# Kernel tuning notes

Measured on AMD Instinct MI355X. Metric: run time of the kernel, lower is better.

The kernel has to match this reference:

```python
import jax, jax.numpy as jnp
import numpy as np

BN_EPS = 1e-3  # Keras BatchNormalization default epsilon


def setup_inputs() -> dict:
    key = jax.random.key(0)
    ks = jax.random.split(key, 16)
    B, N, M = 4, 16384, 4096
    C1, C2 = 128, 256
    mlp = [256, 128]
    cin = C2 + C1
    inp = {
        "xyz1": jax.random.normal(ks[0], (B, N, 3), dtype=jnp.float32),
        "xyz2": jax.random.normal(ks[1], (B, M, 3), dtype=jnp.float32),
        "points1": jax.random.normal(ks[2], (B, N, C1), dtype=jnp.float32),
        "points2": jax.random.normal(ks[3], (B, M, C2), dtype=jnp.float32),
    }
    k = 4
    for i, cout in enumerate(mlp):
        inp[f"w{i}"] = jax.random.normal(ks[k], (cin, cout), dtype=jnp.float32) * (1.0 / np.sqrt(cin)); k += 1
        inp[f"g{i}"] = jnp.ones((cout,), dtype=jnp.float32) + 0.1 * jax.random.normal(ks[k], (cout,), dtype=jnp.float32); k += 1
        inp[f"b{i}"] = 0.1 * jax.random.normal(ks[k], (cout,), dtype=jnp.float32); k += 1
        inp[f"m{i}"] = 0.1 * jax.random.normal(ks[k], (cout,), dtype=jnp.float32); k += 1
        inp[f"v{i}"] = 0.5 + jax.random.uniform(ks[k], (cout,), dtype=jnp.float32); k += 1
        cin = cout
    return inp


def _three_nn(xyz1, xyz2):
    # squared pairwise distances [B,N,M] via ||a||^2 + ||b||^2 - 2ab
    n1 = jnp.sum(xyz1 * xyz1, axis=-1)                      # [B,N]
    n2 = jnp.sum(xyz2 * xyz2, axis=-1)                      # [B,M]
    d2 = n1[:, :, None] + n2[:, None, :] - 2.0 * jnp.einsum("bnc,bmc->bnm", xyz1, xyz2)
    d2 = jnp.maximum(d2, 0.0)
    neg, idx = jax.lax.top_k(-d2, 3)                        # 3 smallest distances
    return -neg, idx                                        # dist [B,N,3], idx [B,N,3]


def reference(xyz1, xyz2, points1, points2,
              w0, g0, b0, m0, v0, w1, g1, b1, m1, v1):
    dist, idx = _three_nn(xyz1, xyz2)
    dist = jnp.maximum(dist, 1e-10)
    inv = 1.0 / dist                                        # [B,N,3]
    weight = inv / jnp.sum(inv, axis=2, keepdims=True)      # [B,N,3]
    # three_interpolate: irregular gather + weighted sum
    gathered = jax.vmap(lambda p, i: p[i])(points2, idx)    # [B,N,3,C2]
    interp = jnp.einsum("bnk,bnkc->bnc", weight, gathered)  # [B,N,C2]
    x = jnp.concatenate([interp, points1], axis=2)          # [B,N,C2+C1]
    # 1x1 Conv2D (no bias) + BN(inference) + ReLU stack
    for w, g, b, m, v in ((w0, g0, b0, m0, v0), (w1, g1, b1, m1, v1)):
        x = jnp.einsum("bnc,cd->bnd", x, w)
        x = (x - m) * (g * jax.lax.rsqrt(v + BN_EPS)) + b
        x = jax.nn.relu(x)
    return x
```

## Files before the change

kernel.cpp:

```cpp
#include <hip/hip_runtime.h>
#include <hip/hip_bf16.h>

typedef __bf16 bf16x8 __attribute__((ext_vector_type(8)));
typedef float  f32x4  __attribute__((ext_vector_type(4)));
typedef unsigned short ushort_t;
typedef unsigned int   uint_t;

__device__ __forceinline__ ushort_t f2bf(float f) {
    union { float f; uint_t u; } v; v.f = f;
    uint_t r = v.u + 0x7fffu + ((v.u >> 16) & 1u);
    return (ushort_t)(r >> 16);
}

__device__ __forceinline__ void async_copy16(const void* g, void* l) {
    __builtin_amdgcn_global_load_lds(
        (const __attribute__((address_space(1))) unsigned int*)g,
        (__attribute__((address_space(3))) unsigned int*)l, 16, 0, 0);
}

#define BATCH 4
#define NPTS  16384
#define MPTS  4096
#define C1    128
#define C2    256
#define NCHUNK 4
#define CHUNK  (MPTS / NCHUNK)

__global__ __launch_bounds__(256) void prep_kernel(
    const float* __restrict__ w0, const float* __restrict__ w1,
    const float* __restrict__ g0, const float* __restrict__ b0,
    const float* __restrict__ m0, const float* __restrict__ v0,
    const float* __restrict__ g1, const float* __restrict__ b1,
    const float* __restrict__ m1, const float* __restrict__ v1,
    ushort_t* __restrict__ wt0, ushort_t* __restrict__ wt1,
    float* __restrict__ sc0, float* __restrict__ sh0,
    float* __restrict__ sc1, float* __restrict__ sh1) {
    int i = blockIdx.x * 256 + threadIdx.x;
    if (i < 256 * 384) {
        int n = i / 384, k = i % 384;
        wt0[i] = f2bf(w0[k * 256 + n]);
    }
    if (i < 128 * 256) {
        int n = i / 256, k = i % 256;
        wt1[i] = f2bf(w1[k * 128 + n]);
    }
    if (i < 256) { float s = g0[i] * rsqrtf(v0[i] + 1e-3f); sc0[i] = s; sh0[i] = b0[i] - m0[i] * s; }
    if (i < 128) { float s = g1[i] * rsqrtf(v1[i] + 1e-3f); sc1[i] = s; sh1[i] = b1[i] - m1[i] * s; }
}

__global__ __launch_bounds__(256) void knn_partial(
    const float* __restrict__ xyz1, const float* __restrict__ xyz2,
    float* __restrict__ pd, int* __restrict__ pi) {
    __shared__ __align__(16) float sx[CHUNK], sy_[CHUNK], sz[CHUNK], sw[CHUNK];
    const int t  = threadIdx.x;
    const int qb = blockIdx.x;
    const int c  = blockIdx.y;
    const int b  = blockIdx.z;
#pragma unroll
    for (int j = 0; j < CHUNK / 256; j++) {
        const int m = j * 256 + t;
        const float* g = xyz2 + ((long)b * MPTS + c * CHUNK + m) * 3;
        const float x = g[0], y = g[1], z = g[2];
        sx[m] = x; sy_[m] = y; sz[m] = z; sw[m] = x * x + y * y + z * z;
    }
    __syncthreads();
    const int n = qb * 256 + t;
    const long base = ((long)b * NPTS + n) * 3;
    const float qx = xyz1[base], qy = xyz1[base + 1], qz = xyz1[base + 2];
    const float nx = -2.f * qx, ny = -2.f * qy, nz = -2.f * qz;
    float d0 = 3.4e38f, d1 = 3.4e38f, d2 = 3.4e38f;
    int   i0 = 0, i1 = 0, i2 = 0;
    const int mb = c * CHUNK;
    for (int g = 0; g < CHUNK; g += 4) {
        const float4 X = *(const float4*)&sx[g];
        const float4 Y = *(const float4*)&sy_[g];
        const float4 Z = *(const float4*)&sz[g];
        const float4 W = *(const float4*)&sw[g];
        const float xs[4] = {X.x, X.y, X.z, X.w};
        const float ys[4] = {Y.x, Y.y, Y.z, Y.w};
        const float zs[4] = {Z.x, Z.y, Z.z, Z.w};
        const float ws[4] = {W.x, W.y, W.z, W.w};
#pragma unroll
        for (int j = 0; j < 4; j++) {
            const float s = fmaf(xs[j], nx, fmaf(ys[j], ny, fmaf(zs[j], nz, ws[j])));
            const int m = mb + g + j;
            const bool c0 = s < d0, c1 = s < d1, c2 = s < d2;
            const int ni2 = c1 ? i1 : (c2 ? m : i2);
            const int ni1 = c0 ? i0 : (c1 ? m : i1);
            const int ni0 = c0 ? m : i0;
            const float nd0 = fminf(d0, s);
            const float nd1 = __builtin_amdgcn_fmed3f(d0, d1, s);
            const float nd2 = __builtin_amdgcn_fmed3f(d1, d2, s);
            d0 = nd0; d1 = nd1; d2 = nd2;
            i0 = ni0; i1 = ni1; i2 = ni2;
        }
    }
    const long po = ((long)c * (BATCH * NPTS) + (long)b * NPTS + n) * 3;
    pd[po] = d0; pd[po + 1] = d1; pd[po + 2] = d2;
    pi[po] = i0; pi[po + 1] = i1; pi[po + 2] = i2;
}

__global__ __launch_bounds__(256) void knn_merge(
    const float* __restrict__ xyz1,
    const float* __restrict__ pd, const int* __restrict__ pi,
    int* __restrict__ idx, float* __restrict__ wgt) {
    const long n = blockIdx.x * 256 + threadIdx.x;
    float d0 = 3.4e38f, d1 = 3.4e38f, d2 = 3.4e38f;
    int   i0 = 0, i1 = 0, i2 = 0;
#pragma unroll
    for (int c = 0; c < NCHUNK; c++) {
        const long po = ((long)c * (BATCH * NPTS) + n) * 3;
#pragma unroll
        for (int k = 0; k < 3; k++) {
            const float d = pd[po + k];
            const int   m = pi[po + k];
            const bool c0 = d < d0, c1 = d < d1, c2 = d < d2;
            const float nd2 = c1 ? d1 : (c2 ? d : d2);
            const int   ni2 = c1 ? i1 : (c2 ? m : i2);
            const float nd1 = c0 ? d0 : (c1 ? d : d1);
            const int   ni1 = c0 ? i0 : (c1 ? m : i1);
            d0 = c0 ? d : d0;  i0 = c0 ? m : i0;
            d1 = nd1; i1 = ni1; d2 = nd2; i2 = ni2;
        }
    }
    const float qx = xyz1[n * 3], qy = xyz1[n * 3 + 1], qz = xyz1[n * 3 + 2];
    const float qn = qx * qx + qy * qy + qz * qz;
    d0 = fmaxf(d0 + qn, 1e-10f);
    d1 = fmaxf(d1 + qn, 1e-10f);
    d2 = fmaxf(d2 + qn, 1e-10f);
    const float w0 = 1.f / d0, w1 = 1.f / d1, w2 = 1.f / d2;
    const float rs = 1.f / (w0 + w1 + w2);
    const long o = n * 3;
    idx[o] = i0; idx[o + 1] = i1; idx[o + 2] = i2;
    wgt[o] = w0 * rs; wgt[o + 1] = w1 * rs; wgt[o + 2] = w2 * rs;
}

__global__ __launch_bounds__(256) void interp_kernel(
    const float* __restrict__ points1, const float* __restrict__ points2,
    const int* __restrict__ idx, const float* __restrict__ wgt,
    ushort_t* __restrict__ x0) {
    const int wave = (blockIdx.x * 256 + threadIdx.x) >> 6;
    const int lane = threadIdx.x & 63;
    const int b = wave >> 14;
    const int n = wave & 16383;
    const long o = (long)wave * 3;
    int i0 = idx[o], i1 = idx[o + 1], i2 = idx[o + 2];
    i0 = min(max(i0, 0), MPTS - 1);
    i1 = min(max(i1, 0), MPTS - 1);
    i2 = min(max(i2, 0), MPTS - 1);
    const float w0 = wgt[o], w1 = wgt[o + 1], w2 = wgt[o + 2];
    const float4* p0 = (const float4*)(points2 + ((long)b * MPTS + i0) * C2);
    const float4* p1 = (const float4*)(points2 + ((long)b * MPTS + i1) * C2);
    const float4* p2 = (const float4*)(points2 + ((long)b * MPTS + i2) * C2);
    float4 a = p0[lane], bb = p1[lane], c = p2[lane];
    ushort4 u;
    u.x = f2bf(w0 * a.x + w1 * bb.x + w2 * c.x);
    u.y = f2bf(w0 * a.y + w1 * bb.y + w2 * c.y);
    u.z = f2bf(w0 * a.z + w1 * bb.z + w2 * c.z);
    u.w = f2bf(w0 * a.w + w1 * bb.w + w2 * c.w);
    ((ushort4*)(x0 + (long)wave * 384))[lane] = u;
    const float2* q = (const float2*)(points1 + ((long)b * NPTS + n) * C1);
    float2 t = q[lane];
    uint_t packed = (uint_t)f2bf(t.x) | ((uint_t)f2bf(t.y) << 16);
    ((uint_t*)(x0 + (long)wave * 384 + 256))[lane] = packed;
}

__global__ __launch_bounds__(256) void mlp_fused(
    const ushort_t* __restrict__ A,
    const ushort_t* __restrict__ Bt0,
    const ushort_t* __restrict__ Bt1,
    const float* __restrict__ sc0, const float* __restrict__ sh0,
    const float* __restrict__ sc1, const float* __restrict__ sh1,
    float* __restrict__ outp) {
    __shared__ ushort_t sA[2048];
    __shared__ ushort_t sB[4096];
    __shared__ ushort_t sy[64 * 264];
    const int tid = threadIdx.x;
    const int wv = tid >> 6, lane = tid & 63;
    const int q = lane >> 4, l16 = lane & 15;
    const int rowBase = blockIdx.x * 64;
    const int wrow = (wv & 1) * 32;
    const int wcol = (wv >> 1) * 64;

#pragma unroll 1
    for (int H = 0; H < 2; H++) {
        f32x4 acc[2][4] = {};
        for (int kk = 0; kk < 384; kk += 32) {
            {
                const int linear = tid * 16;
                const int row = linear >> 6, brow = linear & 63;
                const char* ga = (const char*)A + ((long)(rowBase + row) * 384 + kk) * 2 + brow;
                async_copy16(ga, (char*)sA + wv * 1024);
            }
#pragma unroll
            for (int ch = 0; ch < 2; ch++) {
                const int linear = ch * 4096 + tid * 16;
                const int row = linear >> 6, brow = linear & 63;
                const char* gb = (const char*)Bt0 + ((long)(H * 128 + row) * 384 + kk) * 2 + brow;
                async_copy16(gb, (char*)sB + ch * 4096 + wv * 1024);
            }
            __syncthreads();
            bf16x8 af[2], bfr[4];
#pragma unroll
            for (int t = 0; t < 2; t++)
                af[t] = *(const bf16x8*)((const char*)sA + (wrow + t * 16 + l16) * 64 + q * 16);
#pragma unroll
            for (int t = 0; t < 4; t++)
                bfr[t] = *(const bf16x8*)((const char*)sB + (wcol + t * 16 + l16) * 64 + q * 16);
#pragma unroll
            for (int tr = 0; tr < 2; tr++)
#pragma unroll
                for (int tc = 0; tc < 4; tc++)
                    acc[tr][tc] = __builtin_amdgcn_mfma_f32_16x16x32_bf16(af[tr], bfr[tc], acc[tr][tc], 0, 0, 0);
            __syncthreads();
        }
#pragma unroll
        for (int tc = 0; tc < 4; tc++) {
            const int ycol = H * 128 + wcol + tc * 16 + l16;
            const float sc = sc0[ycol], sh = sh0[ycol];
#pragma unroll
            for (int tr = 0; tr < 2; tr++) {
                const int row0 = wrow + tr * 16 + q * 4;
#pragma unroll
                for (int r = 0; r < 4; r++) {
                    const float v = fmaxf(acc[tr][tc][r] * sc + sh, 0.f);
                    sy[(row0 + r) * 264 + ycol] = f2bf(v);
                }
            }
        }
    }
    __syncthreads();

    f32x4 acc2[2][4] = {};
    for (int kk = 0; kk < 256; kk += 32) {
#pragma unroll
        for (int ch = 0; ch < 2; ch++) {
            const int linear = ch * 4096 + tid * 16;
            const int row = linear >> 6, brow = linear & 63;
            const char* gb = (const char*)Bt1 + ((long)row * 256 + kk) * 2 + brow;
            async_copy16(gb, (char*)sB + ch * 4096 + wv * 1024);
        }
        __syncthreads();
        bf16x8 af2[2], bf2[4];
#pragma unroll
        for (int t = 0; t < 2; t++)
            af2[t] = *(const bf16x8*)((const char*)sy + (wrow + t * 16 + l16) * 528 + kk * 2 + q * 16);
#pragma unroll
        for (int t = 0; t < 4; t++)
            bf2[t] = *(const bf16x8*)((const char*)sB + (wcol + t * 16 + l16) * 64 + q * 16);
#pragma unroll
        for (int tr = 0; tr < 2; tr++)
#pragma unroll
            for (int tc = 0; tc < 4; tc++)
                acc2[tr][tc] = __builtin_amdgcn_mfma_f32_16x16x32_bf16(af2[tr], bf2[tc], acc2[tr][tc], 0, 0, 0);
        __syncthreads();
    }
#pragma unroll
    for (int tc = 0; tc < 4; tc++) {
        const int col = wcol + tc * 16 + l16;
        const float sc = sc1[col], sh = sh1[col];
#pragma unroll
        for (int tr = 0; tr < 2; tr++) {
            const int row0 = rowBase + wrow + tr * 16 + q * 4;
#pragma unroll
            for (int r = 0; r < 4; r++) {
                const float v = fmaxf(acc2[tr][tc][r] * sc + sh, 0.f);
                outp[(long)(row0 + r) * 128 + col] = v;
            }
        }
    }
}

extern "C" void kernel_launch(void* const* d_in, const int* in_sizes, int n_in,
                              void* d_out, int out_size, void* d_ws, size_t ws_size,
                              hipStream_t stream) {
    const float* xyz1    = (const float*)d_in[0];
    const float* xyz2    = (const float*)d_in[1];
    const float* points1 = (const float*)d_in[2];
    const float* points2 = (const float*)d_in[3];
    const float* w0 = (const float*)d_in[4];
    const float* g0 = (const float*)d_in[5];
    const float* b0 = (const float*)d_in[6];
    const float* m0 = (const float*)d_in[7];
    const float* v0 = (const float*)d_in[8];
    const float* w1 = (const float*)d_in[9];
    const float* g1 = (const float*)d_in[10];
    const float* b1 = (const float*)d_in[11];
    const float* m1 = (const float*)d_in[12];
    const float* v1 = (const float*)d_in[13];

    char* ws = (char*)d_ws;
    int*      idx = (int*)ws;
    float*    wgt = (float*)(ws + 786432);
    ushort_t* wt0 = (ushort_t*)(ws + 1572864);
    ushort_t* wt1 = (ushort_t*)(ws + 1769472);
    float*    sc0 = (float*)(ws + 1835008);
    float*    sh0 = sc0 + 256;
    float*    sc1 = sh0 + 256;
    float*    sh1 = sc1 + 128;
    ushort_t* x0  = (ushort_t*)(ws + 2097152);
    float* pd = (float*)(ws + 2097152);
    int*   pi = (int*)(ws + 2097152 + 6291456);

    prep_kernel<<<384, 256, 0, stream>>>(w0, w1, g0, b0, m0, v0, g1, b1, m1, v1,
                                         wt0, wt1, sc0, sh0, sc1, sh1);
    knn_partial<<<dim3(NPTS / 256, NCHUNK, BATCH), 256, 0, stream>>>(xyz1, xyz2, pd, pi);
    knn_merge<<<(BATCH * NPTS) / 256, 256, 0, stream>>>(xyz1, pd, pi, idx, wgt);
    interp_kernel<<<(BATCH * NPTS) / 4, 256, 0, stream>>>(points1, points2, idx, wgt, x0);
    mlp_fused<<<(BATCH * NPTS) / 64, 256, 0, stream>>>(
        x0, wt0, wt1, sc0, sh0, sc1, sh1, (float*)d_out);
}
```

Measured before the change: 282.3 us.

## Fuse interpolation into MLP kernel and add ballot early-skip to KNN scan

The separate interpolation kernel is removed. The MLP kernel now gathers and weights points2 rows directly into a shared-memory tile of 32 rows, which avoids writing and re-reading the bf16 intermediate x0 through global memory. The MLP now reads weight fragments straight from global memory (and L2) instead of staging them in LDS with barriers, and each block handles 32 rows. The KNN partial scan also wraps its top-3 update in a wave-wide ballot, so the insert work is skipped when no lane improves. This adds wave divergence checks and removes weight reuse through LDS.

```diff
diff --git a/kernel.cpp b/kernel.cpp
--- a/kernel.cpp
+++ b/kernel.cpp
@@ -10,12 +10,6 @@
     union { float f; uint_t u; } v; v.f = f;
     uint_t r = v.u + 0x7fffu + ((v.u >> 16) & 1u);
     return (ushort_t)(r >> 16);
-}
-
-__device__ __forceinline__ void async_copy16(const void* g, void* l) {
-    __builtin_amdgcn_global_load_lds(
-        (const __attribute__((address_space(1))) unsigned int*)g,
-        (__attribute__((address_space(3))) unsigned int*)l, 16, 0, 0);
 }
 
 #define BATCH 4
@@ -83,16 +77,19 @@
 #pragma unroll
         for (int j = 0; j < 4; j++) {
             const float s = fmaf(xs[j], nx, fmaf(ys[j], ny, fmaf(zs[j], nz, ws[j])));
-            const int m = mb + g + j;
-            const bool c0 = s < d0, c1 = s < d1, c2 = s < d2;
-            const int ni2 = c1 ? i1 : (c2 ? m : i2);
-            const int ni1 = c0 ? i0 : (c1 ? m : i1);
-            const int ni0 = c0 ? m : i0;
-            const float nd0 = fminf(d0, s);
-            const float nd1 = __builtin_amdgcn_fmed3f(d0, d1, s);
-            const float nd2 = __builtin_amdgcn_fmed3f(d1, d2, s);
-            d0 = nd0; d1 = nd1; d2 = nd2;
-            i0 = ni0; i1 = ni1; i2 = ni2;
+            const bool c2 = s < d2;
+            if (__ballot(c2)) {
+                const int m = mb + g + j;
+                const bool c0 = s < d0, c1 = s < d1;
+                const int ni2 = c1 ? i1 : (c2 ? m : i2);
+                const int ni1 = c0 ? i0 : (c1 ? m : i1);
+                const int ni0 = c0 ? m : i0;
+                const float nd0 = fminf(d0, s);
+                const float nd1 = __builtin_amdgcn_fmed3f(d0, d1, s);
+                const float nd2 = __builtin_amdgcn_fmed3f(d1, d2, s);
+                d0 = nd0; d1 = nd1; d2 = nd2;
+                i0 = ni0; i1 = ni1; i2 = ni2;
+            }
         }
     }
     const long po = ((long)c * (BATCH * NPTS) + (long)b * NPTS + n) * 3;
@@ -135,137 +132,115 @@
     wgt[o] = w0 * rs; wgt[o + 1] = w1 * rs; wgt[o + 2] = w2 * rs;
 }
 
-__global__ __launch_bounds__(256) void interp_kernel(
+#define XT_STRIDE 392
+#define SY_STRIDE 264
+__global__ __launch_bounds__(256) void mlp_fused(
     const float* __restrict__ points1, const float* __restrict__ points2,
     const int* __restrict__ idx, const float* __restrict__ wgt,
-    ushort_t* __restrict__ x0) {
-    const int wave = (blockIdx.x * 256 + threadIdx.x) >> 6;
-    const int lane = threadIdx.x & 63;
-    const int b = wave >> 14;
-    const int n = wave & 16383;
-    const long o = (long)wave * 3;
-    int i0 = idx[o], i1 = idx[o + 1], i2 = idx[o + 2];
-    i0 = min(max(i0, 0), MPTS - 1);
-    i1 = min(max(i1, 0), MPTS - 1);
-    i2 = min(max(i2, 0), MPTS - 1);
-    const float w0 = wgt[o], w1 = wgt[o + 1], w2 = wgt[o + 2];
-    const float4* p0 = (const float4*)(points2 + ((long)b * MPTS + i0) * C2);
-    const float4* p1 = (const float4*)(points2 + ((long)b * MPTS + i1) * C2);
-    const float4* p2 = (const float4*)(points2 + ((long)b * MPTS + i2) * C2);
-    float4 a = p0[lane], bb = p1[lane], c = p2[lane];
-    ushort4 u;
-    u.x = f2bf(w0 * a.x + w1 * bb.x + w2 * c.x);
-    u.y = f2bf(w0 * a.y + w1 * bb.y + w2 * c.y);
-    u.z = f2bf(w0 * a.z + w1 * bb.z + w2 * c.z);
-    u.w = f2bf(w0 * a.w + w1 * bb.w + w2 * c.w);
-    ((ushort4*)(x0 + (long)wave * 384))[lane] = u;
-    const float2* q = (const float2*)(points1 + ((long)b * NPTS + n) * C1);
-    float2 t = q[lane];
-    uint_t packed = (uint_t)f2bf(t.x) | ((uint_t)f2bf(t.y) << 16);
-    ((uint_t*)(x0 + (long)wave * 384 + 256))[lane] = packed;
-}
-
-__global__ __launch_bounds__(256) void mlp_fused(
-    const ushort_t* __restrict__ A,
     const ushort_t* __restrict__ Bt0,
     const ushort_t* __restrict__ Bt1,
     const float* __restrict__ sc0, const float* __restrict__ sh0,
     const float* __restrict__ sc1, const float* __restrict__ sh1,
     float* __restrict__ outp) {
-    __shared__ ushort_t sA[2048];
-    __shared__ ushort_t sB[4096];
-    __shared__ ushort_t sy[64 * 264];
+    __shared__ ushort_t xt[32 * XT_STRIDE];
+    __shared__ ushort_t sy[32 * SY_STRIDE];
     const int tid = threadIdx.x;
     const int wv = tid >> 6, lane = tid & 63;
     const int q = lane >> 4, l16 = lane & 15;
-    const int rowBase = blockIdx.x * 64;
-    const int wrow = (wv & 1) * 32;
-    const int wcol = (wv >> 1) * 64;
-
-#pragma unroll 1
-    for (int H = 0; H < 2; H++) {
-        f32x4 acc[2][4] = {};
-        for (int kk = 0; kk < 384; kk += 32) {
-            {
-                const int linear = tid * 16;
-                const int row = linear >> 6, brow = linear & 63;
-                const char* ga = (const char*)A + ((long)(rowBase + row) * 384 + kk) * 2 + brow;
-                async_copy16(ga, (char*)sA + wv * 1024);
+    const int rowBase = blockIdx.x * 32;
+    const int b = rowBase >> 14;
+
+#pragma unroll
+    for (int rr = 0; rr < 8; rr++) {
+        const int row = wv * 8 + rr;
+        const long o = (long)(rowBase + row) * 3;
+        int i0 = idx[o], i1 = idx[o + 1], i2 = idx[o + 2];
+        i0 = min(max(i0, 0), MPTS - 1);
+        i1 = min(max(i1, 0), MPTS - 1);
+        i2 = min(max(i2, 0), MPTS - 1);
+        const float w0 = wgt[o], w1 = wgt[o + 1], w2 = wgt[o + 2];
+        const float4* p0 = (const float4*)(points2 + ((long)b * MPTS + i0) * C2);
+        const float4* p1 = (const float4*)(points2 + ((long)b * MPTS + i1) * C2);
+        const float4* p2 = (const float4*)(points2 + ((long)b * MPTS + i2) * C2);
+        const float4 a = p0[lane], bb = p1[lane], cc = p2[lane];
+        ushort4 u;
+        u.x = f2bf(w0 * a.x + w1 * bb.x + w2 * cc.x);
+        u.y = f2bf(w0 * a.y + w1 * bb.y + w2 * cc.y);
+        u.z = f2bf(w0 * a.z + w1 * bb.z + w2 * cc.z);
+        u.w = f2bf(w0 * a.w + w1 * bb.w + w2 * cc.w);
+        *(ushort4*)((char*)xt + row * (XT_STRIDE * 2) + lane * 8) = u;
+        const float2* qp = (const float2*)(points1 + (long)(rowBase + row) * C1);
+        const float2 tq = qp[lane];
+        const uint_t packed = (uint_t)f2bf(tq.x) | ((uint_t)f2bf(tq.y) << 16);
+        *(uint_t*)((char*)xt + row * (XT_STRIDE * 2) + 512 + lane * 4) = packed;
+    }
+    __syncthreads();
+
+    const int wcol = wv * 64;
+    f32x4 acc[2][4] = {};
+#pragma unroll 2
+    for (int step = 0; step < 12; step++) {
+        const int kk = step * 32;
+        bf16x8 af[2], bfr[4];
+#pragma unroll
+        for (int t = 0; t < 2; t++)
+            af[t] = *(const bf16x8*)((const char*)xt + (t * 16 + l16) * (XT_STRIDE * 2) + kk * 2 + q * 16);
+#pragma unroll
+        for (int t = 0; t < 4; t++) {
+            const int col = wcol + t * 16 + l16;
+            bfr[t] = *(const bf16x8*)(Bt0 + (long)col * 384 + kk + q * 8);
+        }
+#pragma unroll
+        for (int tr = 0; tr < 2; tr++)
+#pragma unroll
+            for (int tc = 0; tc < 4; tc++)
+                acc[tr][tc] = __builtin_amdgcn_mfma_f32_16x16x32_bf16(af[tr], bfr[tc], acc[tr][tc], 0, 0, 0);
+    }
+#pragma unroll
+    for (int tc = 0; tc < 4; tc++) {
+        const int ycol = wcol + tc * 16 + l16;
+        const float sc = sc0[ycol], sh = sh0[ycol];
+#pragma unroll
+        for (int tr = 0; tr < 2; tr++) {
+#pragma unroll
+            for (int r = 0; r < 4; r++) {
+                const int row0 = tr * 16 + q * 4 + r;
+                sy[row0 * SY_STRIDE + ycol] = f2bf(fmaxf(acc[tr][tc][r] * sc + sh, 0.f));
             }
-#pragma unroll
-            for (int ch = 0; ch < 2; ch++) {
-                const int linear = ch * 4096 + tid * 16;
-                const int row = linear >> 6, brow = linear & 63;
-                const char* gb = (const char*)Bt0 + ((long)(H * 128 + row) * 384 + kk) * 2 + brow;
-                async_copy16(gb, (char*)sB + ch * 4096 + wv * 1024);
-            }
-            __syncthreads();
-            bf16x8 af[2], bfr[4];
-#pragma unroll
-            for (int t = 0; t < 2; t++)
-                af[t] = *(const bf16x8*)((const char*)sA + (wrow + t * 16 + l16) * 64 + q * 16);
-#pragma unroll
-            for (int t = 0; t < 4; t++)
-                bfr[t] = *(const bf16x8*)((const char*)sB + (wcol + t * 16 + l16) * 64 + q * 16);
-#pragma unroll
-            for (int tr = 0; tr < 2; tr++)
-#pragma unroll
-                for (int tc = 0; tc < 4; tc++)
-                    acc[tr][tc] = __builtin_amdgcn_mfma_f32_16x16x32_bf16(af[tr], bfr[tc], acc[tr][tc], 0, 0, 0);
-            __syncthreads();
-        }
-#pragma unroll
-        for (int tc = 0; tc < 4; tc++) {
-            const int ycol = H * 128 + wcol + tc * 16 + l16;
-            const float sc = sc0[ycol], sh = sh0[ycol];
-#pragma unroll
-            for (int tr = 0; tr < 2; tr++) {
-                const int row0 = wrow + tr * 16 + q * 4;
-#pragma unroll
-                for (int r = 0; r < 4; r++) {
-                    const float v = fmaxf(acc[tr][tc][r] * sc + sh, 0.f);
-                    sy[(row0 + r) * 264 + ycol] = f2bf(v);
-                }
-            }
         }
     }
     __syncthreads();
 
-    f32x4 acc2[2][4] = {};
-    for (int kk = 0; kk < 256; kk += 32) {
-#pragma unroll
-        for (int ch = 0; ch < 2; ch++) {
-            const int linear = ch * 4096 + tid * 16;
-            const int row = linear >> 6, brow = linear & 63;
-            const char* gb = (const char*)Bt1 + ((long)row * 256 + kk) * 2 + brow;
-            async_copy16(gb, (char*)sB + ch * 4096 + wv * 1024);
-        }
-        __syncthreads();
-        bf16x8 af2[2], bf2[4];
+    const int wcol2 = wv * 32;
+    f32x4 acc2[2][2] = {};
+#pragma unroll 2
+    for (int step = 0; step < 8; step++) {
+        const int kk = step * 32;
+        bf16x8 af2[2], bf2[2];
 #pragma unroll
         for (int t = 0; t < 2; t++)
-            af2[t] = *(const bf16x8*)((const char*)sy + (wrow + t * 16 + l16) * 528 + kk * 2 + q * 16);
-#pragma unroll
-        for (int t = 0; t < 4; t++)
-            bf2[t] = *(const bf16x8*)((const char*)sB + (wcol + t * 16 + l16) * 64 + q * 16);
+            af2[t] = *(const bf16x8*)((const char*)sy + (t * 16 + l16) * (SY_STRIDE * 2) + kk * 2 + q * 16);
+#pragma unroll
+        for (int t = 0; t < 2; t++) {
+            const int col = wcol2 + t * 16 + l16;
+            bf2[t] = *(const bf16x8*)(Bt1 + (long)col * 256 + kk + q * 8);
+        }
 #pragma unroll
         for (int tr = 0; tr < 2; tr++)
 #pragma unroll
-            for (int tc = 0; tc < 4; tc++)
+            for (int tc = 0; tc < 2; tc++)
                 acc2[tr][tc] = __builtin_amdgcn_mfma_f32_16x16x32_bf16(af2[tr], bf2[tc], acc2[tr][tc], 0, 0, 0);
-        __syncthreads();
-    }
-#pragma unroll
-    for (int tc = 0; tc < 4; tc++) {
-        const int col = wcol + tc * 16 + l16;
+    }
+#pragma unroll
+    for (int tc = 0; tc < 2; tc++) {
+        const int col = wcol2 + tc * 16 + l16;
         const float sc = sc1[col], sh = sh1[col];
 #pragma unroll
         for (int tr = 0; tr < 2; tr++) {
-            const int row0 = rowBase + wrow + tr * 16 + q * 4;
 #pragma unroll
             for (int r = 0; r < 4; r++) {
-                const float v = fmaxf(acc2[tr][tc][r] * sc + sh, 0.f);
-                outp[(long)(row0 + r) * 128 + col] = v;
+                const int row = rowBase + tr * 16 + q * 4 + r;
+                outp[(long)row * 128 + col] = fmaxf(acc2[tr][tc][r] * sc + sh, 0.f);
             }
         }
     }
@@ -298,7 +273,6 @@
     float*    sh0 = sc0 + 256;
     float*    sc1 = sh0 + 256;
     float*    sh1 = sc1 + 128;
-    ushort_t* x0  = (ushort_t*)(ws + 2097152);
     float* pd = (float*)(ws + 2097152);
     int*   pi = (int*)(ws + 2097152 + 6291456);
 
@@ -306,7 +280,6 @@
                                          wt0, wt1, sc0, sh0, sc1, sh1);
     knn_partial<<<dim3(NPTS / 256, NCHUNK, BATCH), 256, 0, stream>>>(xyz1, xyz2, pd, pi);
     knn_merge<<<(BATCH * NPTS) / 256, 256, 0, stream>>>(xyz1, pd, pi, idx, wgt);
-    interp_kernel<<<(BATCH * NPTS) / 4, 256, 0, stream>>>(points1, points2, idx, wgt, x0);
-    mlp_fused<<<(BATCH * NPTS) / 64, 256, 0, stream>>>(
-        x0, wt0, wt1, sc0, sh0, sc1, sh1, (float*)d_out);
-}
+    mlp_fused<<<(BATCH * NPTS) / 32, 256, 0, stream>>>(
+        points1, points2, idx, wgt, wt0, wt1, sc0, sh0, sc1, sh1, (float*)d_out);
+}
```

Result: faster. 269.6 us (-4.5%).
